# Kernel tuning notes

Hardware: AMD Instinct MI355X
Metric: run time of the kernel (lower is better)

## Reference

```python
import jax, jax.numpy as jnp
from jax import lax
import numpy as np

B, T, F = 128, 512, 64
U1_UNITS, U2_UNITS = 256, 128
W_SCALE = 0.05  # keep relu-activated cell state numerically stable


def lstm_relu(x, W, U, b, return_sequences):
    """Keras LSTM with activation='relu', recurrent_activation='sigmoid'.
    x: [B, T, D], W: [D, 4u], U: [u, 4u], b: [4u]. Gate order i, f, g, o.
    Dropout is inactive at inference and omitted."""
    Bsz = x.shape[0]
    units = U.shape[0]

    def step(carry, xt):
        h, c = carry
        z = xt @ W + h @ U + b  # [B, 4u]
        i, f, g, o = jnp.split(z, 4, axis=-1)
        i = jax.nn.sigmoid(i)
        f = jax.nn.sigmoid(f)
        g = jax.nn.relu(g)
        o = jax.nn.sigmoid(o)
        c_new = f * c + i * g
        h_new = o * jax.nn.relu(c_new)
        return (h_new, c_new), h_new

    xs = jnp.swapaxes(x, 0, 1)  # [T, B, D]
    init = (jnp.zeros((Bsz, units), x.dtype), jnp.zeros((Bsz, units), x.dtype))
    (h_last, _), hs = lax.scan(step, init, xs)
    if return_sequences:
        return jnp.swapaxes(hs, 0, 1)  # [B, T, u]
    return h_last  # [B, u]


def setup_inputs() -> dict:
    key = jax.random.key(0)
    ks = jax.random.split(key, 7)
    x = jax.random.normal(ks[0], (B, T, F), dtype=jnp.float32)
    W1 = jax.random.normal(ks[1], (F, 4 * U1_UNITS), dtype=jnp.float32) * W_SCALE
    U1 = jax.random.normal(ks[2], (U1_UNITS, 4 * U1_UNITS), dtype=jnp.float32) * W_SCALE
    b1 = jnp.zeros((4 * U1_UNITS,), dtype=jnp.float32)
    W2 = jax.random.normal(ks[3], (U1_UNITS, 4 * U2_UNITS), dtype=jnp.float32) * W_SCALE
    U2 = jax.random.normal(ks[4], (U2_UNITS, 4 * U2_UNITS), dtype=jnp.float32) * W_SCALE
    b2 = jnp.zeros((4 * U2_UNITS,), dtype=jnp.float32)
    return {"x": x, "W1": W1, "U1": U1, "b1": b1, "W2": W2, "U2": U2, "b2": b2}


def reference(x, W1, U1, b1, W2, U2, b2):
    h_seq = lstm_relu(x, W1, U1, b1, return_sequences=True)   # [B, T, 256]
    out = lstm_relu(h_seq, W2, U2, b2, return_sequences=False)  # [B, 128]
    return out
```

## Files before the change

kernel.cpp:

```cpp
#include <hip/hip_runtime.h>

#define NG 8

__device__ unsigned int g_cnt[NG * 64];

typedef __attribute__((ext_vector_type(8))) short short8;
typedef __attribute__((ext_vector_type(4))) float floatx4;

__device__ __forceinline__ unsigned int split_pack(float v) {
    unsigned int u  = __float_as_uint(v);
    unsigned int hb = u & 0xffff0000u;
    float r = v - __uint_as_float(hb);
    return hb | (__float_as_uint(r) >> 16);
}

__device__ __forceinline__ float sigmoidf_(float z) {
    return 1.0f / (1.0f + __expf(-z));
}

__device__ __forceinline__ void st_coh(unsigned int* p, unsigned int v) {
    __hip_atomic_store(p, v, __ATOMIC_RELAXED, __HIP_MEMORY_SCOPE_AGENT);
}
__device__ __forceinline__ unsigned long long ld_coh64(const unsigned long long* p) {
    return __hip_atomic_load(p, __ATOMIC_RELAXED, __HIP_MEMORY_SCOPE_AGENT);
}

template<int RS, int NJ>
__device__ __forceinline__ void stage_tile(unsigned int* lds, const unsigned int* gsrc, int tid) {
    const unsigned long long* s64 = (const unsigned long long*)gsrc;
    unsigned long long q[NJ];
#pragma unroll
    for (int j = 0; j < NJ; ++j) q[j] = ld_coh64(s64 + tid + 256 * j);
#pragma unroll
    for (int j = 0; j < NJ; ++j) {
        int f   = tid + 256 * j;
        int row = f / (RS / 2);
        int c   = (f % (RS / 2)) * 2;
        *(unsigned long long*)(lds + row * RS + (c ^ ((row & 7) << 2))) = q[j];
    }
}

__device__ __forceinline__ void unpack_lds(const unsigned int* lp, int i0, short8& ah, short8& al) {
    uint4 pa = *(const uint4*)(lp + i0);
    uint4 pb = *(const uint4*)(lp + (i0 ^ 4));
    unsigned int pv[8] = {pa.x, pa.y, pa.z, pa.w, pb.x, pb.y, pb.z, pb.w};
#pragma unroll
    for (int j = 0; j < 8; ++j) {
        ah[j] = (short)(pv[j] >> 16);
        al[j] = (short)(pv[j] & 0xffffu);
    }
}

__device__ __forceinline__ void cvt_x(const float* xp, short8& ah, short8& al) {
    float4 xa = *(const float4*)(xp);
    float4 xb = *(const float4*)(xp + 4);
    float xv[8] = {xa.x, xa.y, xa.z, xa.w, xb.x, xb.y, xb.z, xb.w};
#pragma unroll
    for (int j = 0; j < 8; ++j) {
        unsigned int u  = __float_as_uint(xv[j]);
        unsigned int hb = u & 0xffff0000u;
        float r = xv[j] - __uint_as_float(hb);
        ah[j] = (short)(u >> 16);
        al[j] = (short)(__float_as_uint(r) >> 16);
    }
}

__device__ __forceinline__ void arrive(unsigned int* cnt) {
    __hip_atomic_fetch_add(cnt, 1u, __ATOMIC_RELEASE, __HIP_MEMORY_SCOPE_AGENT);
}
__device__ __forceinline__ void spin_ge(unsigned int* cnt, unsigned int target) {
    while (__hip_atomic_fetch_add(cnt, 0u, __ATOMIC_RELAXED, __HIP_MEMORY_SCOPE_AGENT) < target) {}
}

template<int NKC, int KX, int GW, int UU, bool L1>
__device__ void lstm_role(const float* __restrict__ x,
                          const float* __restrict__ Wm, const float* __restrict__ Um,
                          const float* __restrict__ bias,
                          unsigned int* __restrict__ h1pk, unsigned int* __restrict__ h2pk,
                          float* __restrict__ out,
                          unsigned int* __restrict__ cntA, unsigned int* __restrict__ cntB,
                          int m0, int wid, float (*zex)[17],
                          unsigned int* __restrict__ ldsA, unsigned int* __restrict__ ldsB)
{
    const int tid  = threadIdx.x;
    const int lane = tid & 63;
    const int n    = lane & 15;
    const int quad = lane >> 4;
    const int gate = n >> 2;
    const int u0   = wid * 8;
    const int b_l  = lane >> 2;
    const int ul   = lane & 3;
    const int sw   = (n & 7) << 2;

    short8 bh[2][NKC], bl[2][NKC];
    float bias_v[2];
#pragma unroll
    for (int c = 0; c < 2; ++c) {
        const int col = gate * UU + u0 + c * 4 + (n & 3);
        bias_v[c] = bias[col];
#pragma unroll
        for (int kc = 0; kc < NKC; ++kc) {
#pragma unroll
            for (int j = 0; j < 8; ++j) {
                int k = kc * 32 + quad * 8 + j;
                float w = (k < KX) ? Wm[k * GW + col] : Um[(k - KX) * GW + col];
                unsigned int p = split_pack(w);
                bh[c][kc][j] = (short)(p >> 16);
                bl[c][kc][j] = (short)(p & 0xffffu);
            }
        }
    }

#pragma unroll
    for (int c = 0; c < 2; ++c) {
        if (L1) st_coh(&h1pk[32768 + (m0 + b_l) * 256 + u0 + c * 4 + ul], 0u);
        else    st_coh(&h2pk[16384 + (m0 + b_l) * 128 + u0 + c * 4 + ul], 0u);
    }
    float cst[2] = {0.f, 0.f};

    __syncthreads();
    if (tid == 0) arrive(L1 ? cntA : cntB);

    for (int s = 0; s < 512; ++s) {
        if (tid == 0) {
            if (L1) { spin_ge(cntA, 8u * (s + 1)); if (s >= 2) spin_ge(cntB, 4u * (unsigned)s); }
            else    { spin_ge(cntA, 8u * (s + 2)); spin_ge(cntB, 4u * (s + 1)); }
        }
        __syncthreads();

        if (L1) {
            stage_tile<256, 8>(ldsA, h1pk + ((s + 1) & 1) * 32768 + m0 * 256, tid);
        } else {
            stage_tile<256, 8>(ldsA, h1pk + (s & 1) * 32768 + m0 * 256, tid);
            stage_tile<128, 4>(ldsB, h2pk + ((s + 1) & 1) * 16384 + m0 * 128, tid);
        }
        __syncthreads();

        floatx4 acc[2];
#pragma unroll
        for (int c = 0; c < 2; ++c)
            acc[c] = {bias_v[c], bias_v[c], bias_v[c], bias_v[c]};

        const float* xsrc = L1 ? (x + (size_t)(m0 + n) * (512 * 64) + s * 64) : nullptr;

#pragma unroll
        for (int kc = 0; kc < NKC; ++kc) {
            short8 ah, al;
            if (L1) {
                if (kc < 2) cvt_x(xsrc + kc * 32 + quad * 8, ah, al);
                else        unpack_lds(ldsA, n * 256 + (((kc - 2) * 32 + quad * 8) ^ sw), ah, al);
            } else {
                if (kc < 8) unpack_lds(ldsA, n * 256 + ((kc * 32 + quad * 8) ^ sw), ah, al);
                else        unpack_lds(ldsB, n * 128 + (((kc - 8) * 32 + quad * 8) ^ sw), ah, al);
            }
#pragma unroll
            for (int c = 0; c < 2; ++c) {
                acc[c] = __builtin_amdgcn_mfma_f32_16x16x32_bf16(ah, bh[c][kc], acc[c], 0, 0, 0);
                acc[c] = __builtin_amdgcn_mfma_f32_16x16x32_bf16(ah, bl[c][kc], acc[c], 0, 0, 0);
                acc[c] = __builtin_amdgcn_mfma_f32_16x16x32_bf16(al, bh[c][kc], acc[c], 0, 0, 0);
            }
        }

#pragma unroll
        for (int c = 0; c < 2; ++c) {
#pragma unroll
            for (int r = 0; r < 4; ++r) zex[quad * 4 + r][n] = acc[c][r];
            asm volatile("s_waitcnt lgkmcnt(0)" ::: "memory");
            float zi = zex[b_l][ 0 + ul];
            float zf = zex[b_l][ 4 + ul];
            float zg = zex[b_l][ 8 + ul];
            float zo = zex[b_l][12 + ul];
            asm volatile("s_waitcnt lgkmcnt(0)" ::: "memory");
            float ig = sigmoidf_(zi);
            float fg = sigmoidf_(zf);
            float gg = fmaxf(zg, 0.f);
            float og = sigmoidf_(zo);
            cst[c] = fg * cst[c] + ig * gg;
            float h = og * fmaxf(cst[c], 0.f);
            unsigned int p = split_pack(h);
            int b = m0 + b_l;
            if (L1) {
                st_coh(&h1pk[(s & 1) * 32768 + b * 256 + u0 + c * 4 + ul], p);
            } else {
                st_coh(&h2pk[(s & 1) * 16384 + b * 128 + u0 + c * 4 + ul], p);
                if (s == 511) out[b * 128 + u0 + c * 4 + ul] = h;
            }
        }

        __syncthreads();
        if (tid == 0) arrive(L1 ? cntA : cntB);
    }
}

__global__ void __launch_bounds__(256, 1)
lstm_fused_kernel(const float* __restrict__ x,
                  const float* __restrict__ W1, const float* __restrict__ U1,
                  const float* __restrict__ b1,
                  const float* __restrict__ W2, const float* __restrict__ U2,
                  const float* __restrict__ b2,
                  float* __restrict__ out, unsigned int* __restrict__ ws)
{
    __shared__ float zex[4][16][17];
    __shared__ unsigned int ldsA[16 * 256];
    __shared__ unsigned int ldsB[16 * 128];
    unsigned int* h1pk = ws;
    unsigned int* h2pk = ws + 65536;
    const int g    = blockIdx.x & 7;
    const int role = blockIdx.x >> 3;
    const int wv   = threadIdx.x >> 6;
    const int m0   = g * 16;
    unsigned int* cntA = &g_cnt[g * 64];
    unsigned int* cntB = &g_cnt[g * 64 + 32];
    if (role < 8) {
        lstm_role<10, 64, 1024, 256, true >(x, W1, U1, b1, h1pk, h2pk, out,
                                            cntA, cntB, m0, role * 4 + wv, zex[wv], ldsA, ldsB);
    } else {
        lstm_role<12, 256, 512, 128, false>(x, W2, U2, b2, h1pk, h2pk, out,
                                            cntA, cntB, m0, (role - 8) * 4 + wv, zex[wv], ldsA, ldsB);
    }
}

__global__ void init_kernel(float* __restrict__ out) {
    int t = blockIdx.x * 256 + threadIdx.x;
    if (t < NG * 64) g_cnt[t] = 0u;
    if (t < 16384) out[t] = 7.0f;
}

extern "C" void kernel_launch(void* const* d_in, const int* in_sizes, int n_in,
                              void* d_out, int out_size, void* d_ws, size_t ws_size,
                              hipStream_t stream) {
    const float* x  = (const float*)d_in[0];
    const float* W1 = (const float*)d_in[1];
    const float* U1 = (const float*)d_in[2];
    const float* b1 = (const float*)d_in[3];
    const float* W2 = (const float*)d_in[4];
    const float* U2 = (const float*)d_in[5];
    const float* b2 = (const float*)d_in[6];
    float* out = (float*)d_out;
    unsigned int* ws = (unsigned int*)d_ws;
    init_kernel<<<64, 256, 0, stream>>>(out);
    lstm_fused_kernel<<<96, 256, 0, stream>>>(x, W1, U1, b1, W2, U2, b2, out, ws);
}
```

Measured before the change: 1.961 ms.

## Use per-block arrival flags and hoist input projection before barrier wait

Replaces the two shared per-group counters, which every block incremented atomically, with one flag per block on its own 128-byte slot. Waiters poll all 12 flags in their group and check minimum thresholds. This removes atomic contention on a single counter in exchange for more polling loads. Layer 1 blocks also run the x-projection MFMAs for the step before spinning on the barrier, so that input-dependent work overlaps the wait for the previous hidden state.

```diff
diff --git a/kernel.cpp b/kernel.cpp
--- a/kernel.cpp
+++ b/kernel.cpp
@@ -2,7 +2,7 @@
 
 #define NG 8
 
-__device__ unsigned int g_cnt[NG * 64];
+__device__ __attribute__((aligned(128))) unsigned int g_cnt[NG * 12 * 32];
 
 typedef __attribute__((ext_vector_type(8))) short short8;
 typedef __attribute__((ext_vector_type(4))) float floatx4;
@@ -23,6 +23,29 @@
 }
 __device__ __forceinline__ unsigned long long ld_coh64(const unsigned long long* p) {
     return __hip_atomic_load(p, __ATOMIC_RELAXED, __HIP_MEMORY_SCOPE_AGENT);
+}
+__device__ __forceinline__ unsigned int ld_rmw(unsigned int* p) {
+    return __hip_atomic_fetch_add(p, 0u, __ATOMIC_RELAXED, __HIP_MEMORY_SCOPE_AGENT);
+}
+__device__ __forceinline__ void arrive(unsigned int* flag) {
+    __hip_atomic_fetch_add(flag, 1u, __ATOMIC_RELEASE, __HIP_MEMORY_SCOPE_AGENT);
+}
+
+__device__ __forceinline__ void poll12(unsigned int* fb, unsigned int t1, unsigned int t2) {
+    for (;;) {
+        unsigned int m1 = 0xffffffffu, m2 = 0xffffffffu;
+#pragma unroll
+        for (int r = 0; r < 8; ++r) {
+            unsigned int v = ld_rmw(fb + r * 32);
+            if (v < m1) m1 = v;
+        }
+#pragma unroll
+        for (int r = 8; r < 12; ++r) {
+            unsigned int v = ld_rmw(fb + r * 32);
+            if (v < m2) m2 = v;
+        }
+        if (m1 >= t1 && m2 >= t2) return;
+    }
 }
 
 template<int RS, int NJ>
@@ -65,20 +88,13 @@
     }
 }
 
-__device__ __forceinline__ void arrive(unsigned int* cnt) {
-    __hip_atomic_fetch_add(cnt, 1u, __ATOMIC_RELEASE, __HIP_MEMORY_SCOPE_AGENT);
-}
-__device__ __forceinline__ void spin_ge(unsigned int* cnt, unsigned int target) {
-    while (__hip_atomic_fetch_add(cnt, 0u, __ATOMIC_RELAXED, __HIP_MEMORY_SCOPE_AGENT) < target) {}
-}
-
 template<int NKC, int KX, int GW, int UU, bool L1>
 __device__ void lstm_role(const float* __restrict__ x,
                           const float* __restrict__ Wm, const float* __restrict__ Um,
                           const float* __restrict__ bias,
                           unsigned int* __restrict__ h1pk, unsigned int* __restrict__ h2pk,
                           float* __restrict__ out,
-                          unsigned int* __restrict__ cntA, unsigned int* __restrict__ cntB,
+                          unsigned int* __restrict__ fbase, unsigned int* __restrict__ fown,
                           int m0, int wid, float (*zex)[17],
                           unsigned int* __restrict__ ldsA, unsigned int* __restrict__ ldsB)
 {
@@ -88,6 +104,7 @@
     const int quad = lane >> 4;
     const int gate = n >> 2;
     const int u0   = wid * 8;
+    const int arow = m0 + n;
     const int b_l  = lane >> 2;
     const int ul   = lane & 3;
     const int sw   = (n & 7) << 2;
@@ -119,12 +136,31 @@
     float cst[2] = {0.f, 0.f};
 
     __syncthreads();
-    if (tid == 0) arrive(L1 ? cntA : cntB);
+    if (tid == 0) arrive(fown);
 
     for (int s = 0; s < 512; ++s) {
+        floatx4 acc[2];
+#pragma unroll
+        for (int c = 0; c < 2; ++c)
+            acc[c] = {bias_v[c], bias_v[c], bias_v[c], bias_v[c]};
+        if (L1) {
+            const float* xsrc = x + (size_t)arow * (512 * 64) + s * 64;
+#pragma unroll
+            for (int kc = 0; kc < 2; ++kc) {
+                short8 ah, al;
+                cvt_x(xsrc + kc * 32 + quad * 8, ah, al);
+#pragma unroll
+                for (int c = 0; c < 2; ++c) {
+                    acc[c] = __builtin_amdgcn_mfma_f32_16x16x32_bf16(ah, bh[c][kc], acc[c], 0, 0, 0);
+                    acc[c] = __builtin_amdgcn_mfma_f32_16x16x32_bf16(ah, bl[c][kc], acc[c], 0, 0, 0);
+                    acc[c] = __builtin_amdgcn_mfma_f32_16x16x32_bf16(al, bh[c][kc], acc[c], 0, 0, 0);
+                }
+            }
+        }
+
         if (tid == 0) {
-            if (L1) { spin_ge(cntA, 8u * (s + 1)); if (s >= 2) spin_ge(cntB, 4u * (unsigned)s); }
-            else    { spin_ge(cntA, 8u * (s + 2)); spin_ge(cntB, 4u * (s + 1)); }
+            if (L1) poll12(fbase, (unsigned)(s + 1), (unsigned)s);
+            else    poll12(fbase, (unsigned)(s + 2), (unsigned)(s + 1));
         }
         __syncthreads();
 
@@ -136,23 +172,12 @@
         }
         __syncthreads();
 
-        floatx4 acc[2];
-#pragma unroll
-        for (int c = 0; c < 2; ++c)
-            acc[c] = {bias_v[c], bias_v[c], bias_v[c], bias_v[c]};
-
-        const float* xsrc = L1 ? (x + (size_t)(m0 + n) * (512 * 64) + s * 64) : nullptr;
-
-#pragma unroll
-        for (int kc = 0; kc < NKC; ++kc) {
+#pragma unroll
+        for (int kc = (L1 ? 2 : 0); kc < NKC; ++kc) {
             short8 ah, al;
-            if (L1) {
-                if (kc < 2) cvt_x(xsrc + kc * 32 + quad * 8, ah, al);
-                else        unpack_lds(ldsA, n * 256 + (((kc - 2) * 32 + quad * 8) ^ sw), ah, al);
-            } else {
-                if (kc < 8) unpack_lds(ldsA, n * 256 + ((kc * 32 + quad * 8) ^ sw), ah, al);
-                else        unpack_lds(ldsB, n * 128 + (((kc - 8) * 32 + quad * 8) ^ sw), ah, al);
-            }
+            if (L1)          unpack_lds(ldsA, n * 256 + (((kc - 2) * 32 + quad * 8) ^ sw), ah, al);
+            else if (kc < 8) unpack_lds(ldsA, n * 256 + ((kc * 32 + quad * 8) ^ sw), ah, al);
+            else             unpack_lds(ldsB, n * 128 + (((kc - 8) * 32 + quad * 8) ^ sw), ah, al);
 #pragma unroll
             for (int c = 0; c < 2; ++c) {
                 acc[c] = __builtin_amdgcn_mfma_f32_16x16x32_bf16(ah, bh[c][kc], acc[c], 0, 0, 0);
@@ -188,7 +213,7 @@
         }
 
         __syncthreads();
-        if (tid == 0) arrive(L1 ? cntA : cntB);
+        if (tid == 0) arrive(fown);
     }
 }
 
@@ -209,20 +234,20 @@
     const int role = blockIdx.x >> 3;
     const int wv   = threadIdx.x >> 6;
     const int m0   = g * 16;
-    unsigned int* cntA = &g_cnt[g * 64];
-    unsigned int* cntB = &g_cnt[g * 64 + 32];
+    unsigned int* fbase = &g_cnt[g * 12 * 32];
+    unsigned int* fown  = fbase + role * 32;
     if (role < 8) {
         lstm_role<10, 64, 1024, 256, true >(x, W1, U1, b1, h1pk, h2pk, out,
-                                            cntA, cntB, m0, role * 4 + wv, zex[wv], ldsA, ldsB);
+                                            fbase, fown, m0, role * 4 + wv, zex[wv], ldsA, ldsB);
     } else {
         lstm_role<12, 256, 512, 128, false>(x, W2, U2, b2, h1pk, h2pk, out,
-                                            cntA, cntB, m0, (role - 8) * 4 + wv, zex[wv], ldsA, ldsB);
+                                            fbase, fown, m0, (role - 8) * 4 + wv, zex[wv], ldsA, ldsB);
     }
 }
 
 __global__ void init_kernel(float* __restrict__ out) {
     int t = blockIdx.x * 256 + threadIdx.x;
-    if (t < NG * 64) g_cnt[t] = 0u;
+    if (t < NG * 12 * 32) g_cnt[t] = 0u;
     if (t < 16384) out[t] = 7.0f;
 }
 
```

Result: slower. 3.271 ms (+66.8%).
